# Optimization experiments

Hardware: AMD Instinct MI355X
Metric: run time of the kernel (lower is better)

The kernel has to match this reference:

```python
import jax, jax.numpy as jnp
import numpy as np

EMBED_DIM = 1024
NUM_HEADS = 16
HEAD_DIM = EMBED_DIM // NUM_HEADS


def setup_inputs() -> dict:
    key = jax.random.key(0)
    k1, k2, k3, k4, k5 = jax.random.split(key, 5)
    B, S, D = 2, 2048, EMBED_DIM
    s_in = 1.0 / np.sqrt(D)
    x = jax.random.normal(k1, (B, S, D), dtype=jnp.float32)
    W_qkv = jax.random.uniform(k2, (D, 3 * D), dtype=jnp.float32, minval=-s_in, maxval=s_in)
    b_qkv = jax.random.uniform(k3, (3 * D,), dtype=jnp.float32, minval=-s_in, maxval=s_in)
    W_out = jax.random.uniform(k4, (D, D), dtype=jnp.float32, minval=-s_in, maxval=s_in)
    b_out = jax.random.uniform(k5, (D,), dtype=jnp.float32, minval=-s_in, maxval=s_in)
    return {"x": x, "W_qkv": W_qkv, "b_qkv": b_qkv, "W_out": W_out, "b_out": b_out}


def reference(x, W_qkv, b_qkv, W_out, b_out):
    B, S, D = x.shape
    H, Hd = NUM_HEADS, HEAD_DIM
    qkv = x @ W_qkv + b_qkv                      # [B,S,3D]
    qkv = qkv.reshape(B, S, 3, H, Hd)
    q = qkv[:, :, 0].transpose(0, 2, 1, 3)       # [B,H,S,Hd]
    k = qkv[:, :, 1].transpose(0, 2, 1, 3)
    v = qkv[:, :, 2].transpose(0, 2, 1, 3)
    scores = jnp.einsum('bhsd,bhtd->bhst', q, k) / jnp.sqrt(jnp.float32(Hd))
    attn = jax.nn.softmax(scores, axis=-1)       # dropout is identity in eval mode
    out = jnp.einsum('bhst,bhtd->bhsd', attn, v)
    out = out.transpose(0, 2, 1, 3).reshape(B, S, D)
    return out @ W_out + b_out
```

## Files before the change

kernel.cpp:

```cpp
#include <hip/hip_runtime.h>
#include <stdint.h>
#include <math.h>

#define EMBED 1024
#define HEADS 16
#define HDIM  64
#define SEQ   2048
#define BATCH 2

typedef __bf16 bf16x8 __attribute__((ext_vector_type(8)));
typedef float  f32x4  __attribute__((ext_vector_type(4)));
typedef unsigned short u16x8 __attribute__((ext_vector_type(8)));
typedef unsigned short u16x4 __attribute__((ext_vector_type(4)));
typedef uint32_t u32x4v __attribute__((ext_vector_type(4)));

static __device__ __forceinline__ unsigned short f2bf(float f){
  union { float f; uint32_t u; } v; v.f = f;
  uint32_t u = v.u;
  uint32_t r = (u + 0x7FFFu + ((u >> 16) & 1u)) >> 16;
  return (unsigned short)r;
}
static __device__ __forceinline__ bf16x8 as_bf(u16x8 v){ return __builtin_bit_cast(bf16x8, v); }

static __device__ __forceinline__ uint32_t pk_bf16(float a, float b){
#if defined(__has_builtin) && __has_builtin(__builtin_amdgcn_cvt_pk_bf16_f32)
  typedef __bf16 bf16x2 __attribute__((ext_vector_type(2)));
  bf16x2 p = __builtin_amdgcn_cvt_pk_bf16_f32(a, b);
  return __builtin_bit_cast(uint32_t, p);
#else
  return (uint32_t)f2bf(a) | ((uint32_t)f2bf(b) << 16);
#endif
}

static __device__ __forceinline__ float fexp2(float x){
#if defined(__has_builtin) && __has_builtin(__builtin_amdgcn_exp2f)
  return __builtin_amdgcn_exp2f(x);
#else
  return exp2f(x);
#endif
}

static __device__ __forceinline__ void stage16(const unsigned short* gp,
                                               unsigned short* lp_wave, int lane){
#if defined(__has_builtin) && __has_builtin(__builtin_amdgcn_global_load_lds)
  __builtin_amdgcn_global_load_lds((const __attribute__((address_space(1))) void*)gp,
                                   (__attribute__((address_space(3))) void*)lp_wave,
                                   16, 0, 0);
#else
  *(u16x8*)(lp_wave + lane * 8) = *(const u16x8*)gp;
#endif
}

__global__ __launch_bounds__(256) void prep(
    const float* __restrict__ x,      unsigned short* __restrict__ xb,
    const float* __restrict__ W_qkv,  unsigned short* __restrict__ wqkvT,
    const float* __restrict__ W_out,  unsigned short* __restrict__ woutT)
{
  __shared__ unsigned short T[32 * 36];
  const int bid = blockIdx.x;
  const int t   = threadIdx.x;

  if (bid < 4096){
    int i = (bid * 256 + t) * 4;
    float4 v = *(const float4*)(x + i);
    u16x4 o;
    o[0] = f2bf(v.x); o[1] = f2bf(v.y); o[2] = f2bf(v.z); o[3] = f2bf(v.w);
    *(u16x4*)(xb + i) = o;
    return;
  }
  const float* W; unsigned short* Wt; int N, n0, k0;
  if (bid < 7168){
    int idx = bid - 4096;
    W = W_qkv; Wt = wqkvT; N = 3072;
    n0 = (idx % 96) * 32; k0 = (idx / 96) * 32;
  } else {
    int idx = bid - 7168;
    W = W_out; Wt = woutT; N = 1024;
    n0 = (idx & 31) * 32; k0 = (idx >> 5) * 32;
  }
  int kr = t >> 3, nc = (t & 7) * 4;
  float4 wv = *(const float4*)(W + (size_t)(k0 + kr) * N + n0 + nc);
  T[(nc + 0) * 36 + kr] = f2bf(wv.x);
  T[(nc + 1) * 36 + kr] = f2bf(wv.y);
  T[(nc + 2) * 36 + kr] = f2bf(wv.z);
  T[(nc + 3) * 36 + kr] = f2bf(wv.w);
  __syncthreads();
  int nr = t >> 3, kc = (t & 7) * 4;
  *(u16x4*)(Wt + (size_t)(n0 + nr) * 1024 + k0 + kc) = *(const u16x4*)&T[nr * 36 + kc];
}

__global__ __launch_bounds__(256) void gemm_qkv(
    const unsigned short* __restrict__ A,
    const unsigned short* __restrict__ Bt,
    const float* __restrict__ bias,
    unsigned short* __restrict__ q_ws,
    unsigned short* __restrict__ k_ws,
    unsigned short* __restrict__ vt_ws,
    int M, int N, int K)
{
  __shared__ unsigned short SM[128 * 136];
  unsigned short* As = SM;
  unsigned short* Bs = SM + 8192;
  const int tid  = threadIdx.x;
  const int bm   = blockIdx.x, bn = blockIdx.y;
  const int w    = tid >> 6, lane = tid & 63;
  const int quad = lane >> 4, l16 = lane & 15;
  const int wm   = (w >> 1) * 64, wn = (w & 1) * 64;

  f32x4 acc[4][4] = {};

  for (int k0 = 0; k0 < K; k0 += 64) {
    #pragma unroll
    for (int i = 0; i < 4; i++){
      int c = w * 4 + i;
      int row = c * 8 + (lane >> 3);
      int kg = (lane & 7) ^ (row & 7);
      stage16(A  + (size_t)(bm * 128 + row) * K + k0 + kg * 8, As + c * 512, lane);
      stage16(Bt + (size_t)(bn * 128 + row) * K + k0 + kg * 8, Bs + c * 512, lane);
    }
    __syncthreads();

    #pragma unroll
    for (int kk = 0; kk < 2; kk++){
      bf16x8 af[4], bfr[4];
      #pragma unroll
      for (int t = 0; t < 4; t++){
        int ra = wm + t * 16 + l16;
        int rb = wn + t * 16 + l16;
        af[t]  = as_bf(*(const u16x8*)&As[(ra << 6) + ((((kk << 2) + quad) ^ (ra & 7)) << 3)]);
        bfr[t] = as_bf(*(const u16x8*)&Bs[(rb << 6) + ((((kk << 2) + quad) ^ (rb & 7)) << 3)]);
      }
      #pragma unroll
      for (int mt = 0; mt < 4; mt++)
        #pragma unroll
        for (int nt = 0; nt < 4; nt++)
          acc[mt][nt] = __builtin_amdgcn_mfma_f32_16x16x32_bf16(af[mt], bfr[nt], acc[mt][nt], 0, 0, 0);
    }
    __syncthreads();
  }

  const int which = (bn * 128) >> 10;
  const int b = bm >> 4;
  const int S0 = (bm & 15) * 128;

  if (which == 2){
    #pragma unroll
    for (int nt = 0; nt < 4; nt++){
      int coln = wn + nt * 16 + l16;
      float bv = bias[bn * 128 + coln];
      #pragma unroll
      for (int mt = 0; mt < 4; mt++){
        int sposl = wm + (mt >> 1) * 32 + quad * 8 + (mt & 1) * 4;
        #pragma unroll
        for (int r = 0; r < 4; r++)
          SM[coln * 136 + sposl + r] = f2bf(acc[mt][nt][r] + bv);
      }
    }
  } else {
    const float scale = (which == 0) ? 0.18033688f : 1.0f;
    #pragma unroll
    for (int nt = 0; nt < 4; nt++){
      int coln = wn + nt * 16 + l16;
      float bv = bias[bn * 128 + coln];
      #pragma unroll
      for (int mt = 0; mt < 4; mt++){
        int sl = wm + mt * 16 + quad * 4;
        #pragma unroll
        for (int r = 0; r < 4; r++)
          SM[(sl + r) * 136 + coln] = f2bf((acc[mt][nt][r] + bv) * scale);
      }
    }
  }
  __syncthreads();

  if (which == 2){
    #pragma unroll
    for (int p = 0; p < 8; p++){
      int nl = p * 16 + (tid >> 4);
      int s0 = (tid & 15) * 8;
      u16x8 v = *(const u16x8*)&SM[nl * 136 + s0];
      int ng = bn * 128 + nl;
      int h = (ng & 1023) >> 6, d = ng & 63;
      *(u16x8*)(vt_ws + (size_t)(b * HEADS + h) * SEQ * HDIM + (size_t)d * SEQ + S0 + s0) = v;
    }
  } else {
    unsigned short* dst = (which == 0) ? q_ws : k_ws;
    #pragma unroll
    for (int p = 0; p < 8; p++){
      int sl = p * 16 + (tid >> 4);
      int c0 = (tid & 15) * 8;
      u16x8 v = *(const u16x8*)&SM[sl * 136 + c0];
      int ng = bn * 128 + c0;
      int h = (ng & 1023) >> 6, d = ng & 63;
      *(u16x8*)(dst + (size_t)(b * HEADS + h) * SEQ * HDIM + (size_t)(S0 + sl) * HDIM + d) = v;
    }
  }
}

__global__ __launch_bounds__(256) void gemm_out(
    const unsigned short* __restrict__ A,
    const unsigned short* __restrict__ Bt,
    const float* __restrict__ bias,
    float* __restrict__ Cout,
    int M, int N, int K)
{
  __shared__ unsigned short As[128 * 64];
  __shared__ unsigned short Bs[64 * 64];
  const int tid  = threadIdx.x;
  const int bm   = blockIdx.x, bn = blockIdx.y;
  const int w    = tid >> 6, lane = tid & 63;
  const int quad = lane >> 4, l16 = lane & 15;
  const int wm   = (w >> 1) * 64, wn = (w & 1) * 32;

  f32x4 acc[4][2] = {};

  for (int k0 = 0; k0 < K; k0 += 64) {
    #pragma unroll
    for (int i = 0; i < 4; i++){
      int c = w * 4 + i;
      int row = c * 8 + (lane >> 3);
      int kg = (lane & 7) ^ (row & 7);
      stage16(A + (size_t)(bm * 128 + row) * K + k0 + kg * 8, &As[c * 512], lane);
    }
    #pragma unroll
    for (int i = 0; i < 2; i++){
      int c = w * 2 + i;
      int row = c * 8 + (lane >> 3);
      int kg = (lane & 7) ^ (row & 7);
      stage16(Bt + (size_t)(bn * 64 + row) * K + k0 + kg * 8, &Bs[c * 512], lane);
    }
    __syncthreads();

    #pragma unroll
    for (int kk = 0; kk < 2; kk++){
      bf16x8 af[4], bfr[2];
      #pragma unroll
      for (int t = 0; t < 4; t++){
        int ra = wm + t * 16 + l16;
        af[t] = as_bf(*(const u16x8*)&As[(ra << 6) + ((((kk << 2) + quad) ^ (ra & 7)) << 3)]);
      }
      #pragma unroll
      for (int t = 0; t < 2; t++){
        int rb = wn + t * 16 + l16;
        bfr[t] = as_bf(*(const u16x8*)&Bs[(rb << 6) + ((((kk << 2) + quad) ^ (rb & 7)) << 3)]);
      }
      #pragma unroll
      for (int mt = 0; mt < 4; mt++)
        #pragma unroll
        for (int nt = 0; nt < 2; nt++)
          acc[mt][nt] = __builtin_amdgcn_mfma_f32_16x16x32_bf16(af[mt], bfr[nt], acc[mt][nt], 0, 0, 0);
    }
    __syncthreads();
  }

  #pragma unroll
  for (int mt = 0; mt < 4; mt++)
    #pragma unroll
    for (int nt = 0; nt < 2; nt++)
      #pragma unroll
      for (int r = 0; r < 4; r++){
        int gm = bm * 128 + wm + mt * 16 + quad * 4 + r;
        int gn = bn * 64 + wn + nt * 16 + l16;
        Cout[(size_t)gm * N + gn] = acc[mt][nt][r] + bias[gn];
      }
}

__global__ __launch_bounds__(512) void attn(
    const unsigned short* __restrict__ q_ws,
    const unsigned short* __restrict__ k_ws,
    const unsigned short* __restrict__ vt_ws,
    unsigned short* __restrict__ o_ws)
{
  __shared__ unsigned short Qs[256 * 64];
  __shared__ unsigned short Ks[2][64 * 64];
  __shared__ unsigned short VTs[2][64 * 64];
  const int tid  = threadIdx.x;
  const int wgid = blockIdx.x;
  const int lin  = (wgid & 7) * 32 + (wgid >> 3);
  const int bh   = lin >> 3, qt = lin & 7;
  const int w    = tid >> 6, lane = tid & 63;
  const int quad = lane >> 4, l16 = lane & 15;
  const size_t base = (size_t)bh * SEQ * HDIM;

  #pragma unroll
  for (int i = 0; i < 4; i++){
    int c = w * 4 + i;
    int row = c * 8 + (lane >> 3);
    int kg = (lane & 7) ^ (row & 7);
    stage16(q_ws + base + (size_t)(qt * 256 + row) * HDIM + kg * 8, &Qs[c * 512], lane);
  }

  const int srow = w * 8 + (lane >> 3);
  const int skg  = (lane & 7) ^ (srow & 7);
  const int dofs = w * 512 + lane * 8;

  stage16(k_ws  + base + (size_t)srow * HDIM + skg * 8, &Ks[0][w * 512],  lane);
  stage16(vt_ws + base + (size_t)srow * SEQ + skg * 8,  &VTs[0][w * 512], lane);
  __syncthreads();

  bf16x8 bq[2][2];
  #pragma unroll
  for (int mq = 0; mq < 2; mq++){
    int row = w * 32 + mq * 16 + l16;
    #pragma unroll
    for (int ks = 0; ks < 2; ks++)
      bq[mq][ks] = as_bf(*(const u16x8*)&Qs[(row << 6) + ((((ks << 2) + quad) ^ (row & 7)) << 3)]);
  }

  const unsigned short* kp = k_ws  + base + (size_t)(64 + srow) * HDIM + skg * 8;
  const unsigned short* vp = vt_ws + base + (size_t)srow * SEQ + 64 + skg * 8;

  f32x4 acc[2][4] = {};
  float li[2] = {0.f, 0.f};

  for (int kt2 = 0; kt2 < SEQ / 128; kt2++){
    #pragma unroll
    for (int half = 0; half < 2; half++){
      const int cur = half;
      const int kt  = kt2 * 2 + half;
      u16x8 kpre, vpre;
      if (kt < SEQ / 64 - 1){
        kpre = *(const u16x8*)kp;  kp += 64 * HDIM;
        vpre = *(const u16x8*)vp;  vp += 64;
      }

      f32x4 sf[4][2] = {};
      #pragma unroll
      for (int ks = 0; ks < 2; ks++){
        #pragma unroll
        for (int nt = 0; nt < 4; nt++){
          int rk = nt * 16 + l16;
          bf16x8 ak = as_bf(*(const u16x8*)&Ks[cur][(rk << 6) + ((((ks << 2) + quad) ^ (rk & 7)) << 3)]);
          #pragma unroll
          for (int mq = 0; mq < 2; mq++)
            sf[nt][mq] = __builtin_amdgcn_mfma_f32_16x16x32_bf16(ak, bq[mq][ks], sf[nt][mq], 0, 0, 0);
        }
      }

      #pragma unroll
      for (int nt = 0; nt < 4; nt++)
        #pragma unroll
        for (int mq = 0; mq < 2; mq++)
          #pragma unroll
          for (int r = 0; r < 4; r++)
            sf[nt][mq][r] = fexp2(sf[nt][mq][r]);
      #pragma unroll
      for (int mq = 0; mq < 2; mq++)
        #pragma unroll
        for (int nt = 0; nt < 4; nt++)
          li[mq] += (sf[nt][mq][0] + sf[nt][mq][1]) + (sf[nt][mq][2] + sf[nt][mq][3]);

      #pragma unroll
      for (int c = 0; c < 2; c++){
        bf16x8 ap[2];
        #pragma unroll
        for (int mq = 0; mq < 2; mq++){
          u32x4v aw;
          aw[0] = pk_bf16(sf[c * 2][mq][0],     sf[c * 2][mq][1]);
          aw[1] = pk_bf16(sf[c * 2][mq][2],     sf[c * 2][mq][3]);
          aw[2] = pk_bf16(sf[c * 2 + 1][mq][0], sf[c * 2 + 1][mq][1]);
          aw[3] = pk_bf16(sf[c * 2 + 1][mq][2], sf[c * 2 + 1][mq][3]);
          ap[mq] = __builtin_bit_cast(bf16x8, aw);
        }
        #pragma unroll
        for (int nt = 0; nt < 4; nt++){
          int rv = nt * 16 + l16;
          bf16x8 bv = as_bf(*(const u16x8*)&VTs[cur][(rv << 6) + ((((c << 2) + quad) ^ (rv & 7)) << 3)]);
          #pragma unroll
          for (int mq = 0; mq < 2; mq++)
            acc[mq][nt] = __builtin_amdgcn_mfma_f32_16x16x32_bf16(ap[mq], bv, acc[mq][nt], 0, 0, 0);
        }
      }

      if (kt < SEQ / 64 - 1){
        *(u16x8*)&Ks[cur ^ 1][dofs]  = kpre;
        *(u16x8*)&VTs[cur ^ 1][dofs] = vpre;
      }
      __syncthreads();
    }
  }

  #pragma unroll
  for (int mq = 0; mq < 2; mq++){
    li[mq] += __shfl_xor(li[mq], 16);
    li[mq] += __shfl_xor(li[mq], 32);
  }
  float inv[2] = {1.0f / li[0], 1.0f / li[1]};
  float invr[2][4];
  #pragma unroll
  for (int mq = 0; mq < 2; mq++)
    #pragma unroll
    for (int r = 0; r < 4; r++)
      invr[mq][r] = __shfl(inv[mq], quad * 4 + r);

  int b = bh >> 4, h = bh & 15;
  #pragma unroll
  for (int mq = 0; mq < 2; mq++)
    #pragma unroll
    for (int nt = 0; nt < 4; nt++)
      #pragma unroll
      for (int r = 0; r < 4; r++){
        int s = qt * 256 + w * 32 + mq * 16 + quad * 4 + r;
        int d = h * 64 + nt * 16 + l16;
        o_ws[((size_t)(b * SEQ + s)) * EMBED + d] = f2bf(acc[mq][nt][r] * invr[mq][r]);
      }
}

extern "C" void kernel_launch(void* const* d_in, const int* in_sizes, int n_in,
                              void* d_out, int out_size, void* d_ws, size_t ws_size,
                              hipStream_t stream) {
  const float* x     = (const float*)d_in[0];
  const float* W_qkv = (const float*)d_in[1];
  const float* b_qkv = (const float*)d_in[2];
  const float* W_out = (const float*)d_in[3];
  const float* b_out = (const float*)d_in[4];
  float* out = (float*)d_out;

  char* ws = (char*)d_ws;
  unsigned short* xb    = (unsigned short*)(ws);
  unsigned short* o     = (unsigned short*)(ws);
  unsigned short* q     = (unsigned short*)(ws + ((size_t)8  << 20));
  unsigned short* k     = (unsigned short*)(ws + ((size_t)16 << 20));
  unsigned short* vt    = (unsigned short*)(ws + ((size_t)24 << 20));
  unsigned short* wqkvT = (unsigned short*)(ws + ((size_t)32 << 20));
  unsigned short* woutT = (unsigned short*)(ws + ((size_t)38 << 20));

  prep<<<dim3(8192), dim3(256), 0, stream>>>(x, xb, W_qkv, wqkvT, W_out, woutT);

  gemm_qkv<<<dim3(32, 24), dim3(256), 0, stream>>>(
      xb, wqkvT, b_qkv, q, k, vt, 4096, 3072, 1024);

  attn<<<dim3(256), dim3(512), 0, stream>>>(q, k, vt, o);

  gemm_out<<<dim3(32, 16), dim3(256), 0, stream>>>(
      o, woutT, b_out, out, 4096, 1024, 1024);
}
```

Before: 189.4 us.

## Software-pipeline half the attention waves to overlap softmax with QK MFMA

```diff
diff --git a/kernel.cpp b/kernel.cpp
--- a/kernel.cpp
+++ b/kernel.cpp
@@ -265,7 +265,7 @@
       }
 }
 
-__global__ __launch_bounds__(512) void attn(
+__global__ __launch_bounds__(512, 1) void attn(
     const unsigned short* __restrict__ q_ws,
     const unsigned short* __restrict__ k_ws,
     const unsigned short* __restrict__ vt_ws,
@@ -310,73 +310,167 @@
   const unsigned short* kp = k_ws  + base + (size_t)(64 + srow) * HDIM + skg * 8;
   const unsigned short* vp = vt_ws + base + (size_t)srow * SEQ + 64 + skg * 8;
 
+  const bool grpB = (w >= 4);
+
   f32x4 acc[2][4] = {};
   float li[2] = {0.f, 0.f};
-
-  for (int kt2 = 0; kt2 < SEQ / 128; kt2++){
-    #pragma unroll
-    for (int half = 0; half < 2; half++){
-      const int cur = half;
-      const int kt  = kt2 * 2 + half;
-      u16x8 kpre, vpre;
-      if (kt < SEQ / 64 - 1){
-        kpre = *(const u16x8*)kp;  kp += 64 * HDIM;
-        vpre = *(const u16x8*)vp;  vp += 64;
-      }
-
-      f32x4 sf[4][2] = {};
-      #pragma unroll
-      for (int ks = 0; ks < 2; ks++){
+  f32x4 sf[4][2];
+  bf16x8 bvB[2][4];
+
+  for (int kt = 0; kt < SEQ / 64; kt++){
+    const int cur = kt & 1;
+    const int co  = cur * 4096;
+    u16x8 kpre, vpre;
+    if (kt < SEQ / 64 - 1){
+      kpre = *(const u16x8*)kp;  kp += 64 * HDIM;
+      vpre = *(const u16x8*)vp;  vp += 64;
+    }
+
+    if (!grpB){
+      f32x4 sa[4][2] = {};
+      #pragma unroll
+      for (int ks = 0; ks < 2; ks++)
         #pragma unroll
         for (int nt = 0; nt < 4; nt++){
           int rk = nt * 16 + l16;
-          bf16x8 ak = as_bf(*(const u16x8*)&Ks[cur][(rk << 6) + ((((ks << 2) + quad) ^ (rk & 7)) << 3)]);
+          bf16x8 ak = as_bf(*(const u16x8*)&Ks[0][co + (rk << 6) + ((((ks << 2) + quad) ^ (rk & 7)) << 3)]);
+          #pragma unroll
+          for (int mq = 0; mq < 2; mq++)
+            sa[nt][mq] = __builtin_amdgcn_mfma_f32_16x16x32_bf16(ak, bq[mq][ks], sa[nt][mq], 0, 0, 0);
+        }
+
+      #pragma unroll
+      for (int nt = 0; nt < 4; nt++)
+        #pragma unroll
+        for (int mq = 0; mq < 2; mq++)
+          #pragma unroll
+          for (int r = 0; r < 4; r++)
+            sa[nt][mq][r] = fexp2(sa[nt][mq][r]);
+      #pragma unroll
+      for (int mq = 0; mq < 2; mq++)
+        #pragma unroll
+        for (int nt = 0; nt < 4; nt++)
+          li[mq] += (sa[nt][mq][0] + sa[nt][mq][1]) + (sa[nt][mq][2] + sa[nt][mq][3]);
+
+      #pragma unroll
+      for (int c = 0; c < 2; c++){
+        bf16x8 ap[2];
+        #pragma unroll
+        for (int mq = 0; mq < 2; mq++){
+          u32x4v aw;
+          aw[0] = pk_bf16(sa[c * 2][mq][0],     sa[c * 2][mq][1]);
+          aw[1] = pk_bf16(sa[c * 2][mq][2],     sa[c * 2][mq][3]);
+          aw[2] = pk_bf16(sa[c * 2 + 1][mq][0], sa[c * 2 + 1][mq][1]);
+          aw[3] = pk_bf16(sa[c * 2 + 1][mq][2], sa[c * 2 + 1][mq][3]);
+          ap[mq] = __builtin_bit_cast(bf16x8, aw);
+        }
+        #pragma unroll
+        for (int nt = 0; nt < 4; nt++){
+          int rv = nt * 16 + l16;
+          bf16x8 bv = as_bf(*(const u16x8*)&VTs[0][co + (rv << 6) + ((((c << 2) + quad) ^ (rv & 7)) << 3)]);
+          #pragma unroll
+          for (int mq = 0; mq < 2; mq++)
+            acc[mq][nt] = __builtin_amdgcn_mfma_f32_16x16x32_bf16(ap[mq], bv, acc[mq][nt], 0, 0, 0);
+        }
+      }
+    } else {
+      if (kt > 0){
+        #pragma unroll
+        for (int nt = 0; nt < 4; nt++)
+          #pragma unroll
+          for (int mq = 0; mq < 2; mq++)
+            #pragma unroll
+            for (int r = 0; r < 4; r++)
+              sf[nt][mq][r] = fexp2(sf[nt][mq][r]);
+        #pragma unroll
+        for (int mq = 0; mq < 2; mq++)
+          #pragma unroll
+          for (int nt = 0; nt < 4; nt++)
+            li[mq] += (sf[nt][mq][0] + sf[nt][mq][1]) + (sf[nt][mq][2] + sf[nt][mq][3]);
+
+        #pragma unroll
+        for (int c = 0; c < 2; c++){
+          bf16x8 ap[2];
+          #pragma unroll
+          for (int mq = 0; mq < 2; mq++){
+            u32x4v aw;
+            aw[0] = pk_bf16(sf[c * 2][mq][0],     sf[c * 2][mq][1]);
+            aw[1] = pk_bf16(sf[c * 2][mq][2],     sf[c * 2][mq][3]);
+            aw[2] = pk_bf16(sf[c * 2 + 1][mq][0], sf[c * 2 + 1][mq][1]);
+            aw[3] = pk_bf16(sf[c * 2 + 1][mq][2], sf[c * 2 + 1][mq][3]);
+            ap[mq] = __builtin_bit_cast(bf16x8, aw);
+          }
+          #pragma unroll
+          for (int nt = 0; nt < 4; nt++)
+            #pragma unroll
+            for (int mq = 0; mq < 2; mq++)
+              acc[mq][nt] = __builtin_amdgcn_mfma_f32_16x16x32_bf16(ap[mq], bvB[c][nt], acc[mq][nt], 0, 0, 0);
+        }
+      }
+
+      #pragma unroll
+      for (int nt = 0; nt < 4; nt++)
+        #pragma unroll
+        for (int mq = 0; mq < 2; mq++)
+          sf[nt][mq] = f32x4{0.f, 0.f, 0.f, 0.f};
+      #pragma unroll
+      for (int ks = 0; ks < 2; ks++)
+        #pragma unroll
+        for (int nt = 0; nt < 4; nt++){
+          int rk = nt * 16 + l16;
+          bf16x8 ak = as_bf(*(const u16x8*)&Ks[0][co + (rk << 6) + ((((ks << 2) + quad) ^ (rk & 7)) << 3)]);
           #pragma unroll
           for (int mq = 0; mq < 2; mq++)
             sf[nt][mq] = __builtin_amdgcn_mfma_f32_16x16x32_bf16(ak, bq[mq][ks], sf[nt][mq], 0, 0, 0);
         }
-      }
-
-      #pragma unroll
-      for (int nt = 0; nt < 4; nt++)
-        #pragma unroll
-        for (int mq = 0; mq < 2; mq++)
-          #pragma unroll
-          for (int r = 0; r < 4; r++)
-            sf[nt][mq][r] = fexp2(sf[nt][mq][r]);
-      #pragma unroll
-      for (int mq = 0; mq < 2; mq++)
-        #pragma unroll
-        for (int nt = 0; nt < 4; nt++)
-          li[mq] += (sf[nt][mq][0] + sf[nt][mq][1]) + (sf[nt][mq][2] + sf[nt][mq][3]);
-
-      #pragma unroll
-      for (int c = 0; c < 2; c++){
-        bf16x8 ap[2];
-        #pragma unroll
-        for (int mq = 0; mq < 2; mq++){
-          u32x4v aw;
-          aw[0] = pk_bf16(sf[c * 2][mq][0],     sf[c * 2][mq][1]);
-          aw[1] = pk_bf16(sf[c * 2][mq][2],     sf[c * 2][mq][3]);
-          aw[2] = pk_bf16(sf[c * 2 + 1][mq][0], sf[c * 2 + 1][mq][1]);
-          aw[3] = pk_bf16(sf[c * 2 + 1][mq][2], sf[c * 2 + 1][mq][3]);
-          ap[mq] = __builtin_bit_cast(bf16x8, aw);
-        }
+
+      #pragma unroll
+      for (int c = 0; c < 2; c++)
         #pragma unroll
         for (int nt = 0; nt < 4; nt++){
           int rv = nt * 16 + l16;
-          bf16x8 bv = as_bf(*(const u16x8*)&VTs[cur][(rv << 6) + ((((c << 2) + quad) ^ (rv & 7)) << 3)]);
-          #pragma unroll
-          for (int mq = 0; mq < 2; mq++)
-            acc[mq][nt] = __builtin_amdgcn_mfma_f32_16x16x32_bf16(ap[mq], bv, acc[mq][nt], 0, 0, 0);
+          bvB[c][nt] = as_bf(*(const u16x8*)&VTs[0][co + (rv << 6) + ((((c << 2) + quad) ^ (rv & 7)) << 3)]);
         }
-      }
-
-      if (kt < SEQ / 64 - 1){
-        *(u16x8*)&Ks[cur ^ 1][dofs]  = kpre;
-        *(u16x8*)&VTs[cur ^ 1][dofs] = vpre;
-      }
-      __syncthreads();
+    }
+
+    if (kt < SEQ / 64 - 1){
+      const int no = co ^ 4096;
+      *(u16x8*)&Ks[0][no + dofs]  = kpre;
+      *(u16x8*)&VTs[0][no + dofs] = vpre;
+    }
+    __syncthreads();
+  }
+
+  if (grpB){
+    #pragma unroll
+    for (int nt = 0; nt < 4; nt++)
+      #pragma unroll
+      for (int mq = 0; mq < 2; mq++)
+        #pragma unroll
+        for (int r = 0; r < 4; r++)
+          sf[nt][mq][r] = fexp2(sf[nt][mq][r]);
+    #pragma unroll
+    for (int mq = 0; mq < 2; mq++)
+      #pragma unroll
+      for (int nt = 0; nt < 4; nt++)
+        li[mq] += (sf[nt][mq][0] + sf[nt][mq][1]) + (sf[nt][mq][2] + sf[nt][mq][3]);
+    #pragma unroll
+    for (int c = 0; c < 2; c++){
+      bf16x8 ap[2];
+      #pragma unroll
+      for (int mq = 0; mq < 2; mq++){
+        u32x4v aw;
+        aw[0] = pk_bf16(sf[c * 2][mq][0],     sf[c * 2][mq][1]);
+        aw[1] = pk_bf16(sf[c * 2][mq][2],     sf[c * 2][mq][3]);
+        aw[2] = pk_bf16(sf[c * 2 + 1][mq][0], sf[c * 2 + 1][mq][1]);
+        aw[3] = pk_bf16(sf[c * 2 + 1][mq][2], sf[c * 2 + 1][mq][3]);
+        ap[mq] = __builtin_bit_cast(bf16x8, aw);
+      }
+      #pragma unroll
+      for (int nt = 0; nt < 4; nt++)
+        #pragma unroll
+        for (int mq = 0; mq < 2; mq++)
+          acc[mq][nt] = __builtin_amdgcn_mfma_f32_16x16x32_bf16(ap[mq], bvB[c][nt], acc[mq][nt], 0, 0, 0);
     }
   }
 
```

Result: no change. 187.4 us (-1.0%).
